# Optimization experiments

Hardware: AMD Instinct MI355X
Metric: run time of the kernel (lower is better)

The kernel has to match this reference:

```python
import jax, jax.numpy as jnp
import numpy as np

B, T, C, H = 4, 4096, 1024, 64

def setup_inputs() -> dict:
    key = jax.random.key(0)
    kx, kq, kk, kv = jax.random.split(key, 4)
    # nn.Linear weights are [out, in]; we store them that way and use einsum.
    s = 1.0 / np.sqrt(C)
    return {
        "x": jax.random.normal(kx, (B, T, C), dtype=jnp.float32),
        "Wq": jax.random.uniform(kq, (H, C), dtype=jnp.float32, minval=-s, maxval=s),
        "Wk": jax.random.uniform(kk, (H, C), dtype=jnp.float32, minval=-s, maxval=s),
        "Wv": jax.random.uniform(kv, (H, C), dtype=jnp.float32, minval=-s, maxval=s),
    }

def reference(x, Wq, Wk, Wv):
    # x: [B, T, C]; W*: [H, C] (torch Linear layout)
    Q = jnp.einsum('btc,hc->bth', x, Wq)  # [B, T, H]
    K = jnp.einsum('btc,hc->bth', x, Wk)
    V = jnp.einsum('btc,hc->bth', x, Wv)
    scale = K.shape[-1] ** -0.5
    scores = jnp.einsum('bqh,bkh->bqk', Q, K) * scale  # [B, T, T]
    Tn = x.shape[1]
    causal = jnp.tril(jnp.ones((Tn, Tn), dtype=bool))
    scores = jnp.where(causal, scores, -jnp.inf)
    attn = jax.nn.softmax(scores, axis=-1)
    return jnp.einsum('bqk,bkh->bqh', attn, V)  # [B, T, H]
```

## Files before the change

kernel.cpp:

```cpp
#include <hip/hip_runtime.h>
#include <hip/hip_bf16.h>

#define B_ 4
#define T_ 4096
#define C_ 1024
#define H_ 64

typedef __bf16 bf16x8 __attribute__((ext_vector_type(8)));
typedef float f32x4 __attribute__((ext_vector_type(4)));
typedef unsigned short u16x8 __attribute__((ext_vector_type(8)));

union Frag8 { uint4 u; bf16x8 b; u16x8 s; };

__device__ inline unsigned short bfbits(float f) {
  union { __hip_bfloat16 h; unsigned short u; } cv;
  cv.h = __float2bfloat16(f);
  return cv.u;
}

__device__ inline float b2f(unsigned short u) {
  union { unsigned int i; float f; } c; c.i = ((unsigned int)u) << 16; return c.f;
}

__device__ inline bf16x8 ldb8(const unsigned short* p) {
  Frag8 f; f.u = *(const uint4*)p; return f.b;
}

__device__ inline bf16x8 asbf(uint4 u) { Frag8 f; f.u = u; return f.b; }

__device__ inline Frag8 packA(float4 a0, float4 a1) {
  Frag8 af;
  af.s[0] = bfbits(a0.x); af.s[1] = bfbits(a0.y);
  af.s[2] = bfbits(a0.z); af.s[3] = bfbits(a0.w);
  af.s[4] = bfbits(a1.x); af.s[5] = bfbits(a1.y);
  af.s[6] = bfbits(a1.z); af.s[7] = bfbits(a1.w);
  return af;
}

__device__ inline void gload16(const void* g, void* l) {
  __builtin_amdgcn_global_load_lds(
      (const __attribute__((address_space(1))) unsigned int*)g,
      (__attribute__((address_space(3))) unsigned int*)l, 16, 0, 0);
}

__global__ __launch_bounds__(256) void wconv(const float* __restrict__ Wq,
                                             const float* __restrict__ Wk,
                                             const float* __restrict__ Wv,
                                             unsigned short* __restrict__ Wb) {
  int i = blockIdx.x * 256 + threadIdx.x;
  size_t e = (size_t)i * 4;
  const float* src = (e < 65536) ? (Wq + e)
                   : (e < 131072 ? (Wk + (e - 65536)) : (Wv + (e - 131072)));
  float4 v = *(const float4*)src;
  unsigned long long o =
      (unsigned long long)bfbits(v.x)
    | ((unsigned long long)bfbits(v.y) << 16)
    | ((unsigned long long)bfbits(v.z) << 32)
    | ((unsigned long long)bfbits(v.w) << 48);
  *(unsigned long long*)(Wb + e) = o;
}

__global__ __launch_bounds__(256) void qkv_proj(const float* __restrict__ x,
                                                const unsigned short* __restrict__ Wb,
                                                unsigned short* __restrict__ qkv,
                                                unsigned short* __restrict__ Vt) {
  __shared__ float xs[2048];
  const int lane = threadIdx.x & 63;
  const int wave = threadIdx.x >> 6;
  const int q16 = lane & 15, quad = lane >> 4;
  const size_t row0 = (size_t)blockIdx.x * 32;

  const unsigned short* wp[3];
#pragma unroll
  for (int ct = 0; ct < 3; ++ct) {
    int gcol = wave * 48 + ct * 16;
    wp[ct] = Wb + (size_t)(gcol >> 6) * 65536
                + (size_t)((gcol & 63) + q16) * C_ + quad * 8;
  }

  const int sr = (lane >> 4);
  const int sc_pos = lane & 15;
  f32x4 acc[2][3] = {};

  for (int kc = 0; kc < C_; kc += 64) {
    __syncthreads();
#pragma unroll
    for (int ii = 0; ii < 2; ++ii) {
      int i = wave * 2 + ii;
      int r = i * 4 + sr;
      int sg = (sc_pos >> 1) ^ (r & 7);
      const float* gp = x + (row0 + r) * C_ + kc + sg * 8 + (sc_pos & 1) * 4;
      gload16(gp, &xs[i * 256]);
    }
    uint4 wf[6];
#pragma unroll
    for (int ct = 0; ct < 3; ++ct) {
      wf[ct * 2]     = *(const uint4*)(wp[ct] + kc);
      wf[ct * 2 + 1] = *(const uint4*)(wp[ct] + kc + 32);
    }
    __syncthreads();
#pragma unroll
    for (int s = 0; s < 2; ++s) {
#pragma unroll
      for (int rt = 0; rt < 2; ++rt) {
        int r = rt * 16 + q16;
        int p = ((s * 4 + quad) ^ (r & 7)) * 8;
        const float* ap = &xs[r * 64 + p];
        float4 a0 = *(const float4*)ap;
        float4 a1 = *(const float4*)(ap + 4);
        Frag8 af = packA(a0, a1);
#pragma unroll
        for (int ct = 0; ct < 3; ++ct)
          acc[rt][ct] = __builtin_amdgcn_mfma_f32_16x16x32_bf16(
              af.b, asbf(wf[ct * 2 + s]), acc[rt][ct], 0, 0, 0);
      }
    }
  }

  const int bb = (int)(blockIdx.x >> 7);
#pragma unroll
  for (int rt = 0; rt < 2; ++rt) {
    const int t0 = (int)(row0 - (size_t)bb * T_) + rt * 16 + quad * 4;
#pragma unroll
    for (int ct = 0; ct < 3; ++ct) {
      int gcol = wave * 48 + ct * 16;
      int mat = gcol >> 6, h = (gcol & 63) + q16;
      if (mat == 2) {
        ushort4 v;
        v.x = bfbits(acc[rt][ct][0]); v.y = bfbits(acc[rt][ct][1]);
        v.z = bfbits(acc[rt][ct][2]); v.w = bfbits(acc[rt][ct][3]);
        *(ushort4*)(Vt + ((size_t)bb * H_ + h) * T_ + t0) = v;
      } else {
        float scale = (mat == 0) ? 0.125f : 1.0f;
#pragma unroll
        for (int r = 0; r < 4; ++r) {
          size_t row = row0 + rt * 16 + quad * 4 + r;
          qkv[(size_t)mat * 1048576 + row * H_ + h] = bfbits(acc[rt][ct][r] * scale);
        }
      }
    }
  }
}

__global__ __launch_bounds__(256) void attn(const unsigned short* __restrict__ Q,
                                            const unsigned short* __restrict__ K,
                                            const unsigned short* __restrict__ Vt,
                                            float* __restrict__ part) {
  const int qt = blockIdx.x;
  const int qtl = qt & 255, b = qt >> 8;
  const int ki = (qtl >> 2) + 1;
  const int c = blockIdx.y;
  if (c * 8 >= ki) return;
  const int e = (ki < c * 8 + 8) ? ki : c * 8 + 8;

  __shared__ float ml_s[2][4][16];
  __shared__ float o_s[4][16][68];
  const int lane = threadIdx.x & 63;
  const int wave = threadIdx.x >> 6;
  const int q16 = lane & 15, quad = lane >> 4;

  const unsigned short* Qb = Q + (size_t)b * T_ * H_;
  const unsigned short* Kb = K + (size_t)b * T_ * H_;
  const unsigned short* Vtb = Vt + (size_t)b * H_ * T_;

  const int q0 = qtl * 16;
  bf16x8 qf0 = ldb8(Qb + (size_t)(q0 + q16) * H_ + quad * 8);
  bf16x8 qf1 = ldb8(Qb + (size_t)(q0 + q16) * H_ + 32 + quad * 8);

  f32x4 o0 = {0.f, 0.f, 0.f, 0.f}, o1 = o0, o2 = o0, o3 = o0;
  float m = -3.0e38f, l = 0.0f;

  for (int tl = c * 8 + wave; tl < e; tl += 4) {
    const int kkb = tl * 64;
    uint4 vf[8];
#pragma unroll
    for (int kb2 = 0; kb2 < 2; ++kb2) {
      const unsigned short* vp = Vtb + (size_t)q16 * T_ + kkb + kb2 * 32 + quad * 8;
#pragma unroll
      for (int j = 0; j < 4; ++j)
        vf[kb2 * 4 + j] = *(const uint4*)(vp + (size_t)(16 * j) * T_);
    }
    uint4 kf[8];
#pragma unroll
    for (int kb = 0; kb < 4; ++kb) {
      const unsigned short* kp = Kb + (size_t)(kkb + kb * 16 + q16) * H_ + quad * 8;
      kf[2 * kb]     = *(const uint4*)kp;
      kf[2 * kb + 1] = *(const uint4*)(kp + 32);
    }
    f32x4 st[4];
#pragma unroll
    for (int kb = 0; kb < 4; ++kb) {
      f32x4 s = {0.f, 0.f, 0.f, 0.f};
      s = __builtin_amdgcn_mfma_f32_16x16x32_bf16(asbf(kf[2 * kb]), qf0, s, 0, 0, 0);
      s = __builtin_amdgcn_mfma_f32_16x16x32_bf16(asbf(kf[2 * kb + 1]), qf1, s, 0, 0, 0);
      st[kb] = s;
    }
    if (tl == ki - 1) {
      const int q_abs = q0 + q16;
#pragma unroll
      for (int kb = 0; kb < 4; ++kb)
#pragma unroll
        for (int r = 0; r < 4; ++r) {
          int kk_abs = kkb + kb * 16 + quad * 4 + r;
          if (kk_abs > q_abs) st[kb][r] = -3.0e38f;
        }
    }
    float mloc = fmaxf(fmaxf(st[0][0], st[0][1]), fmaxf(st[0][2], st[0][3]));
#pragma unroll
    for (int kb = 1; kb < 4; ++kb)
      mloc = fmaxf(mloc, fmaxf(fmaxf(st[kb][0], st[kb][1]), fmaxf(st[kb][2], st[kb][3])));
    mloc = fmaxf(mloc, __shfl_xor(mloc, 16));
    mloc = fmaxf(mloc, __shfl_xor(mloc, 32));
    float mnew = fmaxf(m, mloc);
    float alpha = __expf(m - mnew);
    float lsum = 0.f;
    unsigned pk[4][2];
#pragma unroll
    for (int kb = 0; kb < 4; ++kb) {
      float p0 = __expf(st[kb][0] - mnew);
      float p1 = __expf(st[kb][1] - mnew);
      float p2 = __expf(st[kb][2] - mnew);
      float p3 = __expf(st[kb][3] - mnew);
      lsum += (p0 + p1) + (p2 + p3);
      pk[kb][0] = (unsigned)bfbits(p0) | ((unsigned)bfbits(p1) << 16);
      pk[kb][1] = (unsigned)bfbits(p2) | ((unsigned)bfbits(p3) << 16);
    }
    lsum += __shfl_xor(lsum, 16);
    lsum += __shfl_xor(lsum, 32);
    l = l * alpha + lsum;
    m = mnew;
    float ar0 = __shfl(alpha, quad * 4 + 0);
    float ar1 = __shfl(alpha, quad * 4 + 1);
    float ar2 = __shfl(alpha, quad * 4 + 2);
    float ar3 = __shfl(alpha, quad * 4 + 3);
    o0[0] *= ar0; o0[1] *= ar1; o0[2] *= ar2; o0[3] *= ar3;
    o1[0] *= ar0; o1[1] *= ar1; o1[2] *= ar2; o1[3] *= ar3;
    o2[0] *= ar0; o2[1] *= ar1; o2[2] *= ar2; o2[3] *= ar3;
    o3[0] *= ar0; o3[1] *= ar1; o3[2] *= ar2; o3[3] *= ar3;

    const int kbsel = quad >> 1;
    const int src0 = q16 + 32 * (quad & 1);
#pragma unroll
    for (int kb2 = 0; kb2 < 2; ++kb2) {
      int xA = __shfl((int)pk[2 * kb2][0], src0);
      int xB = __shfl((int)pk[2 * kb2 + 1][0], src0);
      int yA = __shfl((int)pk[2 * kb2][1], src0);
      int yB = __shfl((int)pk[2 * kb2 + 1][1], src0);
      int zA = __shfl((int)pk[2 * kb2][0], src0 + 16);
      int zB = __shfl((int)pk[2 * kb2 + 1][0], src0 + 16);
      int wA = __shfl((int)pk[2 * kb2][1], src0 + 16);
      int wB = __shfl((int)pk[2 * kb2 + 1][1], src0 + 16);
      Frag8 pf;
      pf.u.x = (unsigned)(kbsel ? xB : xA);
      pf.u.y = (unsigned)(kbsel ? yB : yA);
      pf.u.z = (unsigned)(kbsel ? zB : zA);
      pf.u.w = (unsigned)(kbsel ? wB : wA);
      o0 = __builtin_amdgcn_mfma_f32_16x16x32_bf16(pf.b, asbf(vf[kb2 * 4 + 0]), o0, 0, 0, 0);
      o1 = __builtin_amdgcn_mfma_f32_16x16x32_bf16(pf.b, asbf(vf[kb2 * 4 + 1]), o1, 0, 0, 0);
      o2 = __builtin_amdgcn_mfma_f32_16x16x32_bf16(pf.b, asbf(vf[kb2 * 4 + 2]), o2, 0, 0, 0);
      o3 = __builtin_amdgcn_mfma_f32_16x16x32_bf16(pf.b, asbf(vf[kb2 * 4 + 3]), o3, 0, 0, 0);
    }
  }

  if (quad == 0) { ml_s[0][wave][q16] = m; ml_s[1][wave][q16] = l; }
  __syncthreads();
  float M = fmaxf(fmaxf(ml_s[0][0][q16], ml_s[0][1][q16]),
                  fmaxf(ml_s[0][2][q16], ml_s[0][3][q16]));
  float beta = __expf(m - M);
  float b0 = __shfl(beta, quad * 4 + 0);
  float b1 = __shfl(beta, quad * 4 + 1);
  float b2 = __shfl(beta, quad * 4 + 2);
  float b3 = __shfl(beta, quad * 4 + 3);
  o0[0] *= b0; o0[1] *= b1; o0[2] *= b2; o0[3] *= b3;
  o1[0] *= b0; o1[1] *= b1; o1[2] *= b2; o1[3] *= b3;
  o2[0] *= b0; o2[1] *= b1; o2[2] *= b2; o2[3] *= b3;
  o3[0] *= b0; o3[1] *= b1; o3[2] *= b2; o3[3] *= b3;
#pragma unroll
  for (int r = 0; r < 4; ++r) {
    o_s[wave][quad * 4 + r][q16 + 0]  = o0[r];
    o_s[wave][quad * 4 + r][q16 + 16] = o1[r];
    o_s[wave][quad * 4 + r][q16 + 32] = o2[r];
    o_s[wave][quad * 4 + r][q16 + 48] = o3[r];
  }
  __syncthreads();

  const int t = threadIdx.x;
  const int row = t >> 4;
  const int col0 = (t & 15) * 4;
  float m0 = ml_s[0][0][row], m1 = ml_s[0][1][row];
  float m2 = ml_s[0][2][row], m3 = ml_s[0][3][row];
  float Mr = fmaxf(fmaxf(m0, m1), fmaxf(m2, m3));
  float lt = ml_s[1][0][row] * __expf(m0 - Mr) + ml_s[1][1][row] * __expf(m1 - Mr)
           + ml_s[1][2][row] * __expf(m2 - Mr) + ml_s[1][3][row] * __expf(m3 - Mr);
  float4 a0 = *(const float4*)&o_s[0][row][col0];
  float4 a1 = *(const float4*)&o_s[1][row][col0];
  float4 a2 = *(const float4*)&o_s[2][row][col0];
  float4 a3 = *(const float4*)&o_s[3][row][col0];
  float* P = part + (size_t)(qt * 8 + c) * 544;
  ushort4 ov;
  ov.x = bfbits(a0.x + a1.x + a2.x + a3.x);
  ov.y = bfbits(a0.y + a1.y + a2.y + a3.y);
  ov.z = bfbits(a0.z + a1.z + a2.z + a3.z);
  ov.w = bfbits(a0.w + a1.w + a2.w + a3.w);
  *((ushort4*)P + t) = ov;
  if ((t & 15) == 0) { P[512 + row] = Mr; P[528 + row] = lt; }
}

__global__ __launch_bounds__(256) void attn_merge(const float* __restrict__ part,
                                                  float* __restrict__ out) {
  const int qt = blockIdx.x;
  const int qtl = qt & 255, b = qt >> 8;
  const int ki = (qtl >> 2) + 1;
  const int nch = (ki + 7) >> 3;
  const int t = threadIdx.x;
  const int row = t >> 4, col0 = (t & 15) * 4;
  const float* P0 = part + (size_t)qt * 8 * 544;
  float M = -3.0e38f;
  for (int c2 = 0; c2 < nch; ++c2) M = fmaxf(M, P0[c2 * 544 + 512 + row]);
  float L = 0.f;
  float ax = 0.f, ay = 0.f, az = 0.f, aw = 0.f;
  for (int c2 = 0; c2 < nch; ++c2) {
    const float* P = P0 + c2 * 544;
    float w = __expf(P[512 + row] - M);
    L += w * P[528 + row];
    ushort4 ov = *((const ushort4*)P + t);
    ax += w * b2f(ov.x); ay += w * b2f(ov.y);
    az += w * b2f(ov.z); aw += w * b2f(ov.w);
  }
  float inv = 1.0f / L;
  float4 r = {ax * inv, ay * inv, az * inv, aw * inv};
  *(float4*)(out + ((size_t)b * T_ + qtl * 16 + row) * H_ + col0) = r;
}

extern "C" void kernel_launch(void* const* d_in, const int* in_sizes, int n_in,
                              void* d_out, int out_size, void* d_ws, size_t ws_size,
                              hipStream_t stream) {
  const float* x  = (const float*)d_in[0];
  const float* Wq = (const float*)d_in[1];
  const float* Wk = (const float*)d_in[2];
  const float* Wv = (const float*)d_in[3];
  float* out = (float*)d_out;
  unsigned short* ws = (unsigned short*)d_ws;

  unsigned short* Wb  = ws;
  unsigned short* qkv = ws + 196608;
  unsigned short* Vt  = qkv + (size_t)2 * 1048576;
  float* part = (float*)(ws + 196608 + (size_t)3 * 1048576);

  wconv<<<192, 256, 0, stream>>>(Wq, Wk, Wv, Wb);
  qkv_proj<<<512, 256, 0, stream>>>(x, Wb, qkv, Vt);
  attn<<<dim3(1024, 8), 256, 0, stream>>>(qkv, qkv + 1048576, Vt, part);
  attn_merge<<<1024, 256, 0, stream>>>(part, out);
}
```

Measured before the change: 195.0 us.

## Unroll attention to two key tiles per wave with single softmax; widen projection K-step

```diff
diff --git a/kernel.cpp b/kernel.cpp
--- a/kernel.cpp
+++ b/kernel.cpp
@@ -27,6 +27,11 @@
 }
 
 __device__ inline bf16x8 asbf(uint4 u) { Frag8 f; f.u = u; return f.b; }
+
+__device__ inline unsigned pkbf(float a, float b) {
+  union { float f; unsigned u; } ua, ub; ua.f = a; ub.f = b;
+  return __builtin_amdgcn_perm(ub.u + 0x8000u, ua.u + 0x8000u, 0x07060302u);
+}
 
 __device__ inline Frag8 packA(float4 a0, float4 a1) {
   Frag8 af;
@@ -41,6 +46,32 @@
   __builtin_amdgcn_global_load_lds(
       (const __attribute__((address_space(1))) unsigned int*)g,
       (__attribute__((address_space(3))) unsigned int*)l, 16, 0, 0);
+}
+
+__device__ inline void pv_tile(const unsigned (*pk)[2], const uint4* vf,
+                               int quad, int src0,
+                               f32x4& o0, f32x4& o1, f32x4& o2, f32x4& o3) {
+  const int kbsel = quad >> 1;
+#pragma unroll
+  for (int kb2 = 0; kb2 < 2; ++kb2) {
+    int xA = __shfl((int)pk[2 * kb2][0], src0);
+    int xB = __shfl((int)pk[2 * kb2 + 1][0], src0);
+    int yA = __shfl((int)pk[2 * kb2][1], src0);
+    int yB = __shfl((int)pk[2 * kb2 + 1][1], src0);
+    int zA = __shfl((int)pk[2 * kb2][0], src0 + 16);
+    int zB = __shfl((int)pk[2 * kb2 + 1][0], src0 + 16);
+    int wA = __shfl((int)pk[2 * kb2][1], src0 + 16);
+    int wB = __shfl((int)pk[2 * kb2 + 1][1], src0 + 16);
+    Frag8 pf;
+    pf.u.x = (unsigned)(kbsel ? xB : xA);
+    pf.u.y = (unsigned)(kbsel ? yB : yA);
+    pf.u.z = (unsigned)(kbsel ? zB : zA);
+    pf.u.w = (unsigned)(kbsel ? wB : wA);
+    o0 = __builtin_amdgcn_mfma_f32_16x16x32_bf16(pf.b, asbf(vf[kb2 * 4 + 0]), o0, 0, 0, 0);
+    o1 = __builtin_amdgcn_mfma_f32_16x16x32_bf16(pf.b, asbf(vf[kb2 * 4 + 1]), o1, 0, 0, 0);
+    o2 = __builtin_amdgcn_mfma_f32_16x16x32_bf16(pf.b, asbf(vf[kb2 * 4 + 2]), o2, 0, 0, 0);
+    o3 = __builtin_amdgcn_mfma_f32_16x16x32_bf16(pf.b, asbf(vf[kb2 * 4 + 3]), o3, 0, 0, 0);
+  }
 }
 
 __global__ __launch_bounds__(256) void wconv(const float* __restrict__ Wq,
@@ -64,7 +95,7 @@
                                                 const unsigned short* __restrict__ Wb,
                                                 unsigned short* __restrict__ qkv,
                                                 unsigned short* __restrict__ Vt) {
-  __shared__ float xs[2048];
+  __shared__ float xs[4096];
   const int lane = threadIdx.x & 63;
   const int wave = threadIdx.x >> 6;
   const int q16 = lane & 15, quad = lane >> 4;
@@ -82,37 +113,38 @@
   const int sc_pos = lane & 15;
   f32x4 acc[2][3] = {};
 
-  for (int kc = 0; kc < C_; kc += 64) {
+  for (int kc = 0; kc < C_; kc += 128) {
     __syncthreads();
 #pragma unroll
-    for (int ii = 0; ii < 2; ++ii) {
-      int i = wave * 2 + ii;
+    for (int ii = 0; ii < 4; ++ii) {
+      int flat = wave * 4 + ii;
+      int h = flat >> 3, i = flat & 7;
       int r = i * 4 + sr;
       int sg = (sc_pos >> 1) ^ (r & 7);
-      const float* gp = x + (row0 + r) * C_ + kc + sg * 8 + (sc_pos & 1) * 4;
-      gload16(gp, &xs[i * 256]);
-    }
-    uint4 wf[6];
-#pragma unroll
-    for (int ct = 0; ct < 3; ++ct) {
-      wf[ct * 2]     = *(const uint4*)(wp[ct] + kc);
-      wf[ct * 2 + 1] = *(const uint4*)(wp[ct] + kc + 32);
-    }
+      const float* gp = x + (row0 + r) * C_ + kc + h * 64 + sg * 8 + (sc_pos & 1) * 4;
+      gload16(gp, &xs[h * 2048 + i * 256]);
+    }
+    uint4 wf[12];
+#pragma unroll
+    for (int ct = 0; ct < 3; ++ct)
+#pragma unroll
+      for (int hs = 0; hs < 4; ++hs)
+        wf[ct * 4 + hs] = *(const uint4*)(wp[ct] + kc + hs * 32);
     __syncthreads();
 #pragma unroll
-    for (int s = 0; s < 2; ++s) {
+    for (int hs = 0; hs < 4; ++hs) {
 #pragma unroll
       for (int rt = 0; rt < 2; ++rt) {
         int r = rt * 16 + q16;
-        int p = ((s * 4 + quad) ^ (r & 7)) * 8;
-        const float* ap = &xs[r * 64 + p];
+        int p = (((hs & 1) * 4 + quad) ^ (r & 7)) * 8;
+        const float* ap = &xs[(hs >> 1) * 2048 + r * 64 + p];
         float4 a0 = *(const float4*)ap;
         float4 a1 = *(const float4*)(ap + 4);
         Frag8 af = packA(a0, a1);
 #pragma unroll
         for (int ct = 0; ct < 3; ++ct)
           acc[rt][ct] = __builtin_amdgcn_mfma_f32_16x16x32_bf16(
-              af.b, asbf(wf[ct * 2 + s]), acc[rt][ct], 0, 0, 0);
+              af.b, asbf(wf[ct * 4 + hs]), acc[rt][ct], 0, 0, 0);
       }
     }
   }
@@ -131,7 +163,7 @@
         v.z = bfbits(acc[rt][ct][2]); v.w = bfbits(acc[rt][ct][3]);
         *(ushort4*)(Vt + ((size_t)bb * H_ + h) * T_ + t0) = v;
       } else {
-        float scale = (mat == 0) ? 0.125f : 1.0f;
+        float scale = (mat == 0) ? 0.18033688f : 1.0f;
 #pragma unroll
         for (int r = 0; r < 4; ++r) {
           size_t row = row0 + rt * 16 + quad * 4 + r;
@@ -167,19 +199,13 @@
   bf16x8 qf0 = ldb8(Qb + (size_t)(q0 + q16) * H_ + quad * 8);
   bf16x8 qf1 = ldb8(Qb + (size_t)(q0 + q16) * H_ + 32 + quad * 8);
 
-  f32x4 o0 = {0.f, 0.f, 0.f, 0.f}, o1 = o0, o2 = o0, o3 = o0;
-  float m = -3.0e38f, l = 0.0f;
-
-  for (int tl = c * 8 + wave; tl < e; tl += 4) {
-    const int kkb = tl * 64;
-    uint4 vf[8];
-#pragma unroll
-    for (int kb2 = 0; kb2 < 2; ++kb2) {
-      const unsigned short* vp = Vtb + (size_t)q16 * T_ + kkb + kb2 * 32 + quad * 8;
-#pragma unroll
-      for (int j = 0; j < 4; ++j)
-        vf[kb2 * 4 + j] = *(const uint4*)(vp + (size_t)(16 * j) * T_);
-    }
+  const int tA = c * 8 + wave;
+  const int tB = tA + 4;
+  const bool vA = tA < e, vB = tB < e;
+
+  f32x4 st[8];
+  {
+    const int kkb = tA * 64;
     uint4 kf[8];
 #pragma unroll
     for (int kb = 0; kb < 4; ++kb) {
@@ -187,7 +213,6 @@
       kf[2 * kb]     = *(const uint4*)kp;
       kf[2 * kb + 1] = *(const uint4*)(kp + 32);
     }
-    f32x4 st[4];
 #pragma unroll
     for (int kb = 0; kb < 4; ++kb) {
       f32x4 s = {0.f, 0.f, 0.f, 0.f};
@@ -195,78 +220,105 @@
       s = __builtin_amdgcn_mfma_f32_16x16x32_bf16(asbf(kf[2 * kb + 1]), qf1, s, 0, 0, 0);
       st[kb] = s;
     }
-    if (tl == ki - 1) {
-      const int q_abs = q0 + q16;
-#pragma unroll
-      for (int kb = 0; kb < 4; ++kb)
-#pragma unroll
-        for (int r = 0; r < 4; ++r) {
-          int kk_abs = kkb + kb * 16 + quad * 4 + r;
-          if (kk_abs > q_abs) st[kb][r] = -3.0e38f;
-        }
-    }
-    float mloc = fmaxf(fmaxf(st[0][0], st[0][1]), fmaxf(st[0][2], st[0][3]));
-#pragma unroll
-    for (int kb = 1; kb < 4; ++kb)
-      mloc = fmaxf(mloc, fmaxf(fmaxf(st[kb][0], st[kb][1]), fmaxf(st[kb][2], st[kb][3])));
-    mloc = fmaxf(mloc, __shfl_xor(mloc, 16));
-    mloc = fmaxf(mloc, __shfl_xor(mloc, 32));
-    float mnew = fmaxf(m, mloc);
-    float alpha = __expf(m - mnew);
-    float lsum = 0.f;
-    unsigned pk[4][2];
+  }
+  {
+    const int kkb = tB * 64;
+    uint4 kf[8];
 #pragma unroll
     for (int kb = 0; kb < 4; ++kb) {
-      float p0 = __expf(st[kb][0] - mnew);
-      float p1 = __expf(st[kb][1] - mnew);
-      float p2 = __expf(st[kb][2] - mnew);
-      float p3 = __expf(st[kb][3] - mnew);
-      lsum += (p0 + p1) + (p2 + p3);
-      pk[kb][0] = (unsigned)bfbits(p0) | ((unsigned)bfbits(p1) << 16);
-      pk[kb][1] = (unsigned)bfbits(p2) | ((unsigned)bfbits(p3) << 16);
-    }
-    lsum += __shfl_xor(lsum, 16);
-    lsum += __shfl_xor(lsum, 32);
-    l = l * alpha + lsum;
-    m = mnew;
-    float ar0 = __shfl(alpha, quad * 4 + 0);
-    float ar1 = __shfl(alpha, quad * 4 + 1);
-    float ar2 = __shfl(alpha, quad * 4 + 2);
-    float ar3 = __shfl(alpha, quad * 4 + 3);
-    o0[0] *= ar0; o0[1] *= ar1; o0[2] *= ar2; o0[3] *= ar3;
-    o1[0] *= ar0; o1[1] *= ar1; o1[2] *= ar2; o1[3] *= ar3;
-    o2[0] *= ar0; o2[1] *= ar1; o2[2] *= ar2; o2[3] *= ar3;
-    o3[0] *= ar0; o3[1] *= ar1; o3[2] *= ar2; o3[3] *= ar3;
-
-    const int kbsel = quad >> 1;
-    const int src0 = q16 + 32 * (quad & 1);
+      const unsigned short* kp = Kb + (size_t)(kkb + kb * 16 + q16) * H_ + quad * 8;
+      kf[2 * kb]     = *(const uint4*)kp;
+      kf[2 * kb + 1] = *(const uint4*)(kp + 32);
+    }
+#pragma unroll
+    for (int kb = 0; kb < 4; ++kb) {
+      f32x4 s = {0.f, 0.f, 0.f, 0.f};
+      s = __builtin_amdgcn_mfma_f32_16x16x32_bf16(asbf(kf[2 * kb]), qf0, s, 0, 0, 0);
+      s = __builtin_amdgcn_mfma_f32_16x16x32_bf16(asbf(kf[2 * kb + 1]), qf1, s, 0, 0, 0);
+      st[4 + kb] = s;
+    }
+  }
+
+  const int q_abs = q0 + q16;
+  if (tA == ki - 1) {
+#pragma unroll
+    for (int kb = 0; kb < 4; ++kb)
+#pragma unroll
+      for (int r = 0; r < 4; ++r)
+        if (tA * 64 + kb * 16 + quad * 4 + r > q_abs) st[kb][r] = -3.0e38f;
+  }
+  if (tB == ki - 1) {
+#pragma unroll
+    for (int kb = 0; kb < 4; ++kb)
+#pragma unroll
+      for (int r = 0; r < 4; ++r)
+        if (tB * 64 + kb * 16 + quad * 4 + r > q_abs) st[4 + kb][r] = -3.0e38f;
+  }
+  if (!vA) {
+#pragma unroll
+    for (int j = 0; j < 4; ++j)
+#pragma unroll
+      for (int r = 0; r < 4; ++r) st[j][r] = -3.0e38f;
+  }
+  if (!vB) {
+#pragma unroll
+    for (int j = 0; j < 4; ++j)
+#pragma unroll
+      for (int r = 0; r < 4; ++r) st[4 + j][r] = -3.0e38f;
+  }
+
+  float m = fmaxf(fmaxf(st[0][0], st[0][1]), fmaxf(st[0][2], st[0][3]));
+#pragma unroll
+  for (int j = 1; j < 8; ++j)
+    m = fmaxf(m, fmaxf(fmaxf(st[j][0], st[j][1]), fmaxf(st[j][2], st[j][3])));
+  m = fmaxf(m, __shfl_xor(m, 16));
+  m = fmaxf(m, __shfl_xor(m, 32));
+
+  uint4 vfA[8];
+#pragma unroll
+  for (int kb2 = 0; kb2 < 2; ++kb2) {
+    const unsigned short* vp = Vtb + (size_t)q16 * T_ + tA * 64 + kb2 * 32 + quad * 8;
+#pragma unroll
+    for (int j = 0; j < 4; ++j)
+      vfA[kb2 * 4 + j] = *(const uint4*)(vp + (size_t)(16 * j) * T_);
+  }
+
+  float lsum = 0.f;
+  unsigned pk[8][2];
+#pragma unroll
+  for (int j = 0; j < 8; ++j) {
+    float p0 = exp2f(st[j][0] - m);
+    float p1 = exp2f(st[j][1] - m);
+    float p2 = exp2f(st[j][2] - m);
+    float p3 = exp2f(st[j][3] - m);
+    lsum += (p0 + p1) + (p2 + p3);
+    pk[j][0] = pkbf(p0, p1);
+    pk[j][1] = pkbf(p2, p3);
+  }
+  lsum += __shfl_xor(lsum, 16);
+  lsum += __shfl_xor(lsum, 32);
+  const float l = lsum;
+
+  f32x4 o0 = {0.f, 0.f, 0.f, 0.f}, o1 = o0, o2 = o0, o3 = o0;
+  const int src0 = q16 + 32 * (quad & 1);
+  if (vA) pv_tile(&pk[0], vfA, quad, src0, o0, o1, o2, o3);
+  if (vB) {
+    uint4 vfB[8];
 #pragma unroll
     for (int kb2 = 0; kb2 < 2; ++kb2) {
-      int xA = __shfl((int)pk[2 * kb2][0], src0);
-      int xB = __shfl((int)pk[2 * kb2 + 1][0], src0);
-      int yA = __shfl((int)pk[2 * kb2][1], src0);
-      int yB = __shfl((int)pk[2 * kb2 + 1][1], src0);
-      int zA = __shfl((int)pk[2 * kb2][0], src0 + 16);
-      int zB = __shfl((int)pk[2 * kb2 + 1][0], src0 + 16);
-      int wA = __shfl((int)pk[2 * kb2][1], src0 + 16);
-      int wB = __shfl((int)pk[2 * kb2 + 1][1], src0 + 16);
-      Frag8 pf;
-      pf.u.x = (unsigned)(kbsel ? xB : xA);
-      pf.u.y = (unsigned)(kbsel ? yB : yA);
-      pf.u.z = (unsigned)(kbsel ? zB : zA);
-      pf.u.w = (unsigned)(kbsel ? wB : wA);
-      o0 = __builtin_amdgcn_mfma_f32_16x16x32_bf16(pf.b, asbf(vf[kb2 * 4 + 0]), o0, 0, 0, 0);
-      o1 = __builtin_amdgcn_mfma_f32_16x16x32_bf16(pf.b, asbf(vf[kb2 * 4 + 1]), o1, 0, 0, 0);
-      o2 = __builtin_amdgcn_mfma_f32_16x16x32_bf16(pf.b, asbf(vf[kb2 * 4 + 2]), o2, 0, 0, 0);
-      o3 = __builtin_amdgcn_mfma_f32_16x16x32_bf16(pf.b, asbf(vf[kb2 * 4 + 3]), o3, 0, 0, 0);
-    }
+      const unsigned short* vp = Vtb + (size_t)q16 * T_ + tB * 64 + kb2 * 32 + quad * 8;
+#pragma unroll
+      for (int j = 0; j < 4; ++j)
+        vfB[kb2 * 4 + j] = *(const uint4*)(vp + (size_t)(16 * j) * T_);
+    }
+    pv_tile(&pk[4], vfB, quad, src0, o0, o1, o2, o3);
   }
 
   if (quad == 0) { ml_s[0][wave][q16] = m; ml_s[1][wave][q16] = l; }
   __syncthreads();
   float M = fmaxf(fmaxf(ml_s[0][0][q16], ml_s[0][1][q16]),
                   fmaxf(ml_s[0][2][q16], ml_s[0][3][q16]));
-  float beta = __expf(m - M);
+  float beta = exp2f(m - M);
   float b0 = __shfl(beta, quad * 4 + 0);
   float b1 = __shfl(beta, quad * 4 + 1);
   float b2 = __shfl(beta, quad * 4 + 2);
@@ -290,8 +342,8 @@
   float m0 = ml_s[0][0][row], m1 = ml_s[0][1][row];
   float m2 = ml_s[0][2][row], m3 = ml_s[0][3][row];
   float Mr = fmaxf(fmaxf(m0, m1), fmaxf(m2, m3));
-  float lt = ml_s[1][0][row] * __expf(m0 - Mr) + ml_s[1][1][row] * __expf(m1 - Mr)
-           + ml_s[1][2][row] * __expf(m2 - Mr) + ml_s[1][3][row] * __expf(m3 - Mr);
+  float lt = ml_s[1][0][row] * exp2f(m0 - Mr) + ml_s[1][1][row] * exp2f(m1 - Mr)
+           + ml_s[1][2][row] * exp2f(m2 - Mr) + ml_s[1][3][row] * exp2f(m3 - Mr);
   float4 a0 = *(const float4*)&o_s[0][row][col0];
   float4 a1 = *(const float4*)&o_s[1][row][col0];
   float4 a2 = *(const float4*)&o_s[2][row][col0];
@@ -321,7 +373,7 @@
   float ax = 0.f, ay = 0.f, az = 0.f, aw = 0.f;
   for (int c2 = 0; c2 < nch; ++c2) {
     const float* P = P0 + c2 * 544;
-    float w = __expf(P[512 + row] - M);
+    float w = exp2f(P[512 + row] - M);
     L += w * P[528 + row];
     ushort4 ov = *((const ushort4*)P + t);
     ax += w * b2f(ov.x); ay += w * b2f(ov.y);
```

New measurement: 196.9 us. About the same (+1.0%).
